# Kernel tuning notes

Hardware: AMD Instinct MI355X
Metric: run time of the kernel (lower is better)

Reference implementation:

```python
import jax, jax.numpy as jnp
import numpy as np


def setup_inputs() -> dict:
    key = jax.random.key(0)
    ks = jax.random.split(key, 6)
    b, t, k, h = 2, 2048, 256, 8
    s = 1.0 / np.sqrt(k)
    return {
        "x": jax.random.normal(ks[0], (b, t, k), dtype=jnp.float32),
        "Wq": jax.random.normal(ks[1], (k, k * h), dtype=jnp.float32) * s,
        "Wk": jax.random.normal(ks[2], (k, k * h), dtype=jnp.float32) * s,
        "Wv": jax.random.normal(ks[3], (k, k * h), dtype=jnp.float32) * s,
        "Wu": jax.random.normal(ks[4], (k * h, k), dtype=jnp.float32) * (1.0 / np.sqrt(k * h)),
        "bu": jnp.zeros((k,), dtype=jnp.float32),
    }


def reference(x, Wq, Wk, Wv, Wu, bu):
    b, t, k = x.shape
    h = Wq.shape[1] // k
    scale = k ** (-0.25)
    # projections -> [b, t, h, k] -> [b, h, t, k]
    q = (x @ Wq).reshape(b, t, h, k).transpose(0, 2, 1, 3) * scale
    kk = (x @ Wk).reshape(b, t, h, k).transpose(0, 2, 1, 3) * scale
    v = (x @ Wv).reshape(b, t, h, k).transpose(0, 2, 1, 3)
    dot = jnp.einsum('bhqk,bhsk->bhqs', q, kk)  # [b,h,t,t]
    attn = jax.nn.softmax(dot, axis=-1)
    out = jnp.einsum('bhqs,bhsk->bhqk', attn, v)  # [b,h,t,k]
    out = out.transpose(0, 2, 1, 3).reshape(b, t, h * k)
    return out @ Wu + bu
```

## Files before the change

kernel.cpp:

```cpp
#include <hip/hip_runtime.h>

using bf16x8   = __bf16 __attribute__((ext_vector_type(8)));
using floatx4  = float __attribute__((ext_vector_type(4)));
using floatx16 = float __attribute__((ext_vector_type(16)));

static __device__ __forceinline__ unsigned short f2b(float x) {
  unsigned u = __builtin_bit_cast(unsigned, x);
  u = (u + 0x7fffu + ((u >> 16) & 1u)) >> 16;
  return (unsigned short)u;
}

static __device__ __forceinline__ void gl_lds16(const unsigned short* g, unsigned short* l) {
  __builtin_amdgcn_global_load_lds((const __attribute__((address_space(1))) void*)g,
                                   (__attribute__((address_space(3))) void*)l, 16, 0, 0);
}

__global__ __launch_bounds__(256) void prep_kernel(const float* __restrict__ x,
                                                   const float* __restrict__ Wq,
                                                   const float* __restrict__ Wk,
                                                   const float* __restrict__ Wv,
                                                   const float* __restrict__ Wu,
                                                   unsigned short* __restrict__ xb,
                                                   unsigned short* __restrict__ wqkt,
                                                   unsigned short* __restrict__ wvt,
                                                   unsigned short* __restrict__ wut) {
  int bx = blockIdx.x;
  if (bx < 1024) {
    int i = (bx * 256 + threadIdx.x) * 4;
    float4 v = *(const float4*)(x + i);
    unsigned long long p = (unsigned long long)f2b(v.x) |
                           ((unsigned long long)f2b(v.y) << 16) |
                           ((unsigned long long)f2b(v.z) << 32) |
                           ((unsigned long long)f2b(v.w) << 48);
    *(unsigned long long*)(xb + i) = p;
    return;
  }
  __shared__ unsigned short T[64][65];
  const float* src;
  unsigned short* dst;
  int R, C, tile;
  if (bx < 1152)      { src = Wq; dst = wqkt;          R = 256;  C = 2048; tile = bx - 1024; }
  else if (bx < 1280) { src = Wk; dst = wqkt + 524288; R = 256;  C = 2048; tile = bx - 1152; }
  else if (bx < 1408) { src = Wv; dst = wvt;           R = 256;  C = 2048; tile = bx - 1280; }
  else                { src = Wu; dst = wut;           R = 2048; C = 256;  tile = bx - 1408; }
  int ctiles = C >> 6;
  int cx = tile % ctiles, ry = tile / ctiles;
  int r0 = ry * 64, c0 = cx * 64;
  int t = threadIdx.x;
#pragma unroll
  for (int i = 0; i < 16; ++i) {
    int idx = i * 256 + t;
    int r = idx >> 6, c = idx & 63;
    T[r][c] = f2b(src[(size_t)(r0 + r) * C + c0 + c]);
  }
  __syncthreads();
#pragma unroll
  for (int i = 0; i < 16; ++i) {
    int idx = i * 256 + t;
    int c = idx >> 6, r = idx & 63;
    dst[(size_t)(c0 + c) * R + r0 + r] = T[r][c];
  }
}

__global__ __launch_bounds__(256) void proj_kernel(const unsigned short* __restrict__ A,
                                                   const unsigned short* __restrict__ Bt,
                                                   unsigned short* __restrict__ qkb,
                                                   unsigned short* __restrict__ vtb) {
  __shared__ __align__(16) unsigned short SMEM[128 * 136];
  unsigned short* As = SMEM;
  unsigned short* Bs = SMEM + 4096;
  const int Kt = 256;
  int tid = threadIdx.x, lane = tid & 63, w = tid >> 6;
  int m16 = lane & 15, quad = lane >> 4;
  int wr = w & 1, wc = w >> 1;
  int m0 = blockIdx.y * 128, n0 = blockIdx.x * 128;
  int srow0 = w * 32 + (lane >> 2);
  int schunk = (lane & 3) ^ ((lane >> 2) & 3);
  floatx4 acc[4][4] = {};
  for (int k0 = 0; k0 < Kt; k0 += 32) {
    __syncthreads();
#pragma unroll
    for (int j = 0; j < 2; ++j) {
      int r = srow0 + j * 16;
      gl_lds16(A + (size_t)(m0 + r) * Kt + k0 + schunk * 8, &As[(w * 32 + j * 16) * 32]);
      gl_lds16(Bt + (size_t)(n0 + r) * Kt + k0 + schunk * 8, &Bs[(w * 32 + j * 16) * 32]);
    }
    __syncthreads();
    int sw = (quad ^ (m16 & 3)) * 8;
    bf16x8 af[4], bfr[4];
#pragma unroll
    for (int i = 0; i < 4; ++i) {
      af[i]  = *(const bf16x8*)(&As[(wr * 64 + i * 16 + m16) * 32 + sw]);
      bfr[i] = *(const bf16x8*)(&Bs[(wc * 64 + i * 16 + m16) * 32 + sw]);
    }
#pragma unroll
    for (int i = 0; i < 4; ++i)
#pragma unroll
      for (int jn = 0; jn < 4; ++jn)
        acc[i][jn] = __builtin_amdgcn_mfma_f32_16x16x32_bf16(af[i], bfr[jn], acc[i][jn], 0, 0, 0);
  }
  if (n0 < 4096) {
    float qscale = (n0 < 2048) ? 0.0625f : 1.0f;
#pragma unroll
    for (int i = 0; i < 4; ++i)
#pragma unroll
      for (int jn = 0; jn < 4; ++jn)
#pragma unroll
        for (int r = 0; r < 4; ++r) {
          int m = m0 + wr * 64 + i * 16 + quad * 4 + r;
          int n = n0 + wc * 64 + jn * 16 + m16;
          qkb[(size_t)m * 4096 + n] = f2b(acc[i][jn][r] * qscale);
        }
  } else {
    __syncthreads();
    unsigned short* Vt = SMEM;
#pragma unroll
    for (int i = 0; i < 4; ++i)
#pragma unroll
      for (int jn = 0; jn < 4; ++jn)
#pragma unroll
        for (int r = 0; r < 4; ++r) {
          int nn = wc * 64 + jn * 16 + m16;
          int mm = wr * 64 + i * 16 + quad * 4 + r;
          Vt[nn * 136 + mm] = f2b(acc[i][jn][r]);
        }
    __syncthreads();
    int bb = m0 >> 11, t0 = m0 & 2047;
#pragma unroll
    for (int i2 = 0; i2 < 8; ++i2) {
      int idx = i2 * 256 + tid;
      int nn = idx >> 4;
      int mc = (idx & 15) * 8;
      uint4 v = *(const uint4*)(&Vt[nn * 136 + mc]);
      *(uint4*)(&vtb[((size_t)(bb * 2048 + n0 - 4096 + nn)) * 2048 + t0 + mc]) = v;
    }
  }
}

__global__ __launch_bounds__(256) void out_kernel(const unsigned short* __restrict__ A,
                                                  const unsigned short* __restrict__ Bt,
                                                  float* __restrict__ Cout,
                                                  const float* __restrict__ bias) {
  __shared__ unsigned short As[64 * 128];
  __shared__ unsigned short Bs[64 * 128];
  const int Kt = 2048;
  int tid = threadIdx.x, lane = tid & 63, w = tid >> 6;
  int m16 = lane & 15, quad = lane >> 4;
  int m0 = blockIdx.y * 64, n0 = blockIdx.x * 64;
  int srow_i = lane >> 4;
  int spos = lane & 15;
  int rsw = m16 & 7;
  floatx4 acc[4] = {};
  for (int k0 = 0; k0 < Kt; k0 += 128) {
    __syncthreads();
#pragma unroll
    for (int j = 0; j < 4; ++j) {
      int r = w * 16 + j * 4 + srow_i;
      gl_lds16(A + (size_t)(m0 + r) * Kt + k0 + ((spos ^ (r & 7)) * 8), &As[(w * 16 + j * 4) * 128]);
      gl_lds16(Bt + (size_t)(n0 + r) * Kt + k0 + ((spos ^ (r & 7)) * 8), &Bs[(w * 16 + j * 4) * 128]);
    }
    __syncthreads();
    bf16x8 af[4];
#pragma unroll
    for (int kk = 0; kk < 4; ++kk)
      af[kk] = *(const bf16x8*)(&As[(w * 16 + m16) * 128 + (((kk * 4 + quad) ^ rsw) * 8)]);
#pragma unroll
    for (int nt = 0; nt < 4; ++nt)
#pragma unroll
      for (int kk = 0; kk < 4; ++kk) {
        bf16x8 bfv = *(const bf16x8*)(&Bs[(nt * 16 + m16) * 128 + (((kk * 4 + quad) ^ rsw) * 8)]);
        acc[nt] = __builtin_amdgcn_mfma_f32_16x16x32_bf16(af[kk], bfv, acc[nt], 0, 0, 0);
      }
  }
#pragma unroll
  for (int nt = 0; nt < 4; ++nt)
#pragma unroll
    for (int r = 0; r < 4; ++r) {
      int m = m0 + w * 16 + quad * 4 + r;
      int n = n0 + nt * 16 + m16;
      Cout[(size_t)m * 256 + n] = acc[nt][r] + bias[n];
    }
}

__global__ __launch_bounds__(512, 2) void attn_kernel(const unsigned short* __restrict__ qk,
                                                      const unsigned short* __restrict__ vt,
                                                      unsigned short* __restrict__ ao) {
  __shared__ __align__(16) unsigned short Ks[2][64 * 256];
  __shared__ __align__(16) unsigned short Vs[2][256 * 64];
  __shared__ __align__(16) unsigned short Pb[4][32 * 72];
  int tid = threadIdx.x, lane = tid & 63, w = tid >> 6;
  int c32 = lane & 31, hi = lane >> 5;
  int qg = w & 3, u = w >> 2;
  int id = blockIdx.x;
  int xcd = id & 7, j = id >> 3;
  int bh = xcd + 8 * (j & 1);
  int q0 = (j >> 1) * 128;
  int b = bh >> 3, h = bh & 7;

  bf16x8 qf[16];
  const unsigned short* qrow =
      qk + (size_t)(b * 2048 + q0 + qg * 32 + c32) * 4096 + h * 256 + hi * 8;
#pragma unroll
  for (int kk = 0; kk < 16; ++kk) qf[kk] = *(const bf16x8*)(qrow + kk * 16);

  bf16x8 onesf;
#pragma unroll
  for (int i = 0; i < 8; ++i) onesf[i] = (__bf16)1.0f;

  floatx16 O[4] = {};
  floatx16 l = {};

  const unsigned short* kbase = qk + (size_t)b * 2048 * 4096 + 2048 + h * 256;
  const unsigned short* vbase = vt + (size_t)bh * 256 * 2048;
  unsigned short* pq = &Pb[qg][0];

  int krow_i = lane >> 5, kpos = lane & 31;
  int vrow_i = lane >> 3, vpos = lane & 7;
  int ksw = c32 & 7;

#pragma unroll
  for (int i = 0; i < 4; ++i) {
    int kr = i * 2 + krow_i;
    gl_lds16(kbase + (size_t)(w * 8 + kr) * 4096 + ((kpos ^ (kr & 7)) * 8),
             &Ks[0][(w * 8 + i * 2) * 256]);
    int vr = i * 8 + vrow_i;
    gl_lds16(vbase + (size_t)(w * 32 + vr) * 2048 + ((vpos ^ vrow_i) * 8),
             &Vs[0][(w * 32 + i * 8) * 64]);
  }

  for (int st = 0; st < 32; ++st) {
    int cur = st & 1;
    __syncthreads();

    floatx16 s = {};
    const unsigned short* krl = &Ks[cur][(u * 32 + c32) * 256];
#pragma unroll
    for (int kk = 0; kk < 16; ++kk) {
      bf16x8 kf = *(const bf16x8*)(krl + (((kk * 2 + hi) ^ ksw) * 8));
      s = __builtin_amdgcn_mfma_f32_32x32x16_bf16(qf[kk], kf, s, 0, 0, 0);
    }
#pragma unroll
    for (int i = 0; i < 16; ++i) {
      float p = __expf(s[i]);
      int q = (i & 3) + 8 * (i >> 2) + 4 * hi;
      pq[q * 72 + u * 32 + c32] = f2b(p);
    }
    __syncthreads();

    if (st < 31) {
      int s0 = (st + 1) * 64;
      unsigned short* kdst = &Ks[1 - cur][0];
      unsigned short* vdst = &Vs[1 - cur][0];
#pragma unroll
      for (int i = 0; i < 4; ++i) {
        int kr = i * 2 + krow_i;
        gl_lds16(kbase + (size_t)(s0 + w * 8 + kr) * 4096 + ((kpos ^ (kr & 7)) * 8),
                 kdst + (w * 8 + i * 2) * 256);
        int vr = i * 8 + vrow_i;
        gl_lds16(vbase + (size_t)(w * 32 + vr) * 2048 + s0 + ((vpos ^ vrow_i) * 8),
                 vdst + (w * 32 + i * 8) * 64);
      }
    }

    bf16x8 paf[4];
#pragma unroll
    for (int f = 0; f < 4; ++f) paf[f] = *(const bf16x8*)(pq + c32 * 72 + f * 16 + hi * 8);
#pragma unroll
    for (int f = 0; f < 4; ++f)
      l = __builtin_amdgcn_mfma_f32_32x32x16_bf16(paf[f], onesf, l, 0, 0, 0);
#pragma unroll
    for (int dt = 0; dt < 4; ++dt) {
      const unsigned short* vrl = &Vs[cur][(u * 128 + dt * 32 + c32) * 64];
#pragma unroll
      for (int f = 0; f < 4; ++f) {
        bf16x8 vf = *(const bf16x8*)(vrl + (((f * 2 + hi) ^ ksw) * 8));
        O[dt] = __builtin_amdgcn_mfma_f32_32x32x16_bf16(paf[f], vf, O[dt], 0, 0, 0);
      }
    }
  }
  float inv[16];
#pragma unroll
  for (int i = 0; i < 16; ++i) inv[i] = 1.0f / l[i];
#pragma unroll
  for (int dt = 0; dt < 4; ++dt)
#pragma unroll
    for (int i = 0; i < 16; ++i) {
      int q = (i & 3) + 8 * (i >> 2) + 4 * hi;
      ao[(size_t)(b * 2048 + q0 + qg * 32 + q) * 2048 + h * 256 + u * 128 + dt * 32 + c32] =
          f2b(O[dt][i] * inv[i]);
    }
}

extern "C" void kernel_launch(void* const* d_in, const int* in_sizes, int n_in,
                              void* d_out, int out_size, void* d_ws, size_t ws_size,
                              hipStream_t stream) {
  const float* x  = (const float*)d_in[0];
  const float* Wq = (const float*)d_in[1];
  const float* Wk = (const float*)d_in[2];
  const float* Wv = (const float*)d_in[3];
  const float* Wu = (const float*)d_in[4];
  const float* bu = (const float*)d_in[5];

  unsigned short* xb   = (unsigned short*)d_ws;
  unsigned short* wqkt = xb + 1048576;
  unsigned short* wvt  = wqkt + 1048576;
  unsigned short* wut  = wvt + 524288;
  unsigned short* qkb  = wut + 524288;
  unsigned short* vtb  = qkb + 16777216;
  unsigned short* aob  = vtb + 8388608;

  prep_kernel<<<1536, 256, 0, stream>>>(x, Wq, Wk, Wv, Wu, xb, wqkt, wvt, wut);
  proj_kernel<<<dim3(48, 32), 256, 0, stream>>>(xb, wqkt, qkb, vtb);
  attn_kernel<<<256, 512, 0, stream>>>(qkb, vtb, aob);
  out_kernel<<<dim3(4, 64), 256, 0, stream>>>(aob, wut, (float*)d_out, bu);
}
```

Baseline: 193.7 us.

## Double-buffer LDS in projection/output GEMMs and compute softmax denominators with scalar sums

Both GEMM kernels now double-buffer the shared-memory tiles. The next k-slab is prefetched with global_load_lds while MFMAs run on the current slab, which removes one barrier per iteration. In the attention kernel, the row-sum MFMA against a ones vector is replaced by per-lane fp32 accumulation of the exponentials. This is followed by a cross-lane shuffle reduction and an LDS exchange between the two key-halves at the end. This drops 4 MFMAs per step and uses unrounded fp32 sums, at the cost of more LDS and extra final synchronisation.

New measurement: 191.6 us. No clear change (-1.1%).

```diff
diff --git a/kernel.cpp b/kernel.cpp
--- a/kernel.cpp
+++ b/kernel.cpp
@@ -67,8 +67,6 @@
                                                    unsigned short* __restrict__ qkb,
                                                    unsigned short* __restrict__ vtb) {
   __shared__ __align__(16) unsigned short SMEM[128 * 136];
-  unsigned short* As = SMEM;
-  unsigned short* Bs = SMEM + 4096;
   const int Kt = 256;
   int tid = threadIdx.x, lane = tid & 63, w = tid >> 6;
   int m16 = lane & 15, quad = lane >> 4;
@@ -77,15 +75,27 @@
   int srow0 = w * 32 + (lane >> 2);
   int schunk = (lane & 3) ^ ((lane >> 2) & 3);
   floatx4 acc[4][4] = {};
+#pragma unroll
+  for (int j = 0; j < 2; ++j) {
+    int r = srow0 + j * 16;
+    gl_lds16(A + (size_t)(m0 + r) * Kt + schunk * 8, &SMEM[(w * 32 + j * 16) * 32]);
+    gl_lds16(Bt + (size_t)(n0 + r) * Kt + schunk * 8, &SMEM[4096 + (w * 32 + j * 16) * 32]);
+  }
   for (int k0 = 0; k0 < Kt; k0 += 32) {
-    __syncthreads();
-#pragma unroll
-    for (int j = 0; j < 2; ++j) {
-      int r = srow0 + j * 16;
-      gl_lds16(A + (size_t)(m0 + r) * Kt + k0 + schunk * 8, &As[(w * 32 + j * 16) * 32]);
-      gl_lds16(Bt + (size_t)(n0 + r) * Kt + k0 + schunk * 8, &Bs[(w * 32 + j * 16) * 32]);
-    }
-    __syncthreads();
+    int cur = (k0 >> 5) & 1;
+    unsigned short* As = SMEM + cur * 8192;
+    unsigned short* Bs = As + 4096;
+    __syncthreads();
+    if (k0 + 32 < Kt) {
+      unsigned short* Ad = SMEM + (1 - cur) * 8192;
+      unsigned short* Bd = Ad + 4096;
+#pragma unroll
+      for (int j = 0; j < 2; ++j) {
+        int r = srow0 + j * 16;
+        gl_lds16(A + (size_t)(m0 + r) * Kt + k0 + 32 + schunk * 8, Ad + (w * 32 + j * 16) * 32);
+        gl_lds16(Bt + (size_t)(n0 + r) * Kt + k0 + 32 + schunk * 8, Bd + (w * 32 + j * 16) * 32);
+      }
+    }
     int sw = (quad ^ (m16 & 3)) * 8;
     bf16x8 af[4], bfr[4];
 #pragma unroll
@@ -141,8 +151,7 @@
                                                   const unsigned short* __restrict__ Bt,
                                                   float* __restrict__ Cout,
                                                   const float* __restrict__ bias) {
-  __shared__ unsigned short As[64 * 128];
-  __shared__ unsigned short Bs[64 * 128];
+  __shared__ __align__(16) unsigned short SMEM[32768];
   const int Kt = 2048;
   int tid = threadIdx.x, lane = tid & 63, w = tid >> 6;
   int m16 = lane & 15, quad = lane >> 4;
@@ -151,15 +160,29 @@
   int spos = lane & 15;
   int rsw = m16 & 7;
   floatx4 acc[4] = {};
+#pragma unroll
+  for (int j = 0; j < 4; ++j) {
+    int r = w * 16 + j * 4 + srow_i;
+    gl_lds16(A + (size_t)(m0 + r) * Kt + ((spos ^ (r & 7)) * 8), &SMEM[(w * 16 + j * 4) * 128]);
+    gl_lds16(Bt + (size_t)(n0 + r) * Kt + ((spos ^ (r & 7)) * 8), &SMEM[8192 + (w * 16 + j * 4) * 128]);
+  }
   for (int k0 = 0; k0 < Kt; k0 += 128) {
-    __syncthreads();
-#pragma unroll
-    for (int j = 0; j < 4; ++j) {
-      int r = w * 16 + j * 4 + srow_i;
-      gl_lds16(A + (size_t)(m0 + r) * Kt + k0 + ((spos ^ (r & 7)) * 8), &As[(w * 16 + j * 4) * 128]);
-      gl_lds16(Bt + (size_t)(n0 + r) * Kt + k0 + ((spos ^ (r & 7)) * 8), &Bs[(w * 16 + j * 4) * 128]);
-    }
-    __syncthreads();
+    int cur = (k0 >> 7) & 1;
+    unsigned short* As = SMEM + cur * 16384;
+    unsigned short* Bs = As + 8192;
+    __syncthreads();
+    if (k0 + 128 < Kt) {
+      unsigned short* Ad = SMEM + (1 - cur) * 16384;
+      unsigned short* Bd = Ad + 8192;
+#pragma unroll
+      for (int j = 0; j < 4; ++j) {
+        int r = w * 16 + j * 4 + srow_i;
+        gl_lds16(A + (size_t)(m0 + r) * Kt + k0 + 128 + ((spos ^ (r & 7)) * 8),
+                 Ad + (w * 16 + j * 4) * 128);
+        gl_lds16(Bt + (size_t)(n0 + r) * Kt + k0 + 128 + ((spos ^ (r & 7)) * 8),
+                 Bd + (w * 16 + j * 4) * 128);
+      }
+    }
     bf16x8 af[4];
 #pragma unroll
     for (int kk = 0; kk < 4; ++kk)
@@ -203,12 +226,8 @@
 #pragma unroll
   for (int kk = 0; kk < 16; ++kk) qf[kk] = *(const bf16x8*)(qrow + kk * 16);
 
-  bf16x8 onesf;
-#pragma unroll
-  for (int i = 0; i < 8; ++i) onesf[i] = (__bf16)1.0f;
-
   floatx16 O[4] = {};
-  floatx16 l = {};
+  floatx16 lacc = {};
 
   const unsigned short* kbase = qk + (size_t)b * 2048 * 4096 + 2048 + h * 256;
   const unsigned short* vbase = vt + (size_t)bh * 256 * 2048;
@@ -242,6 +261,7 @@
 #pragma unroll
     for (int i = 0; i < 16; ++i) {
       float p = __expf(s[i]);
+      lacc[i] += p;
       int q = (i & 3) + 8 * (i >> 2) + 4 * hi;
       pq[q * 72 + u * 32 + c32] = f2b(p);
     }
@@ -266,9 +286,6 @@
 #pragma unroll
     for (int f = 0; f < 4; ++f) paf[f] = *(const bf16x8*)(pq + c32 * 72 + f * 16 + hi * 8);
 #pragma unroll
-    for (int f = 0; f < 4; ++f)
-      l = __builtin_amdgcn_mfma_f32_32x32x16_bf16(paf[f], onesf, l, 0, 0, 0);
-#pragma unroll
     for (int dt = 0; dt < 4; ++dt) {
       const unsigned short* vrl = &Vs[cur][(u * 128 + dt * 32 + c32) * 64];
 #pragma unroll
@@ -278,16 +295,29 @@
       }
     }
   }
-  float inv[16];
-#pragma unroll
-  for (int i = 0; i < 16; ++i) inv[i] = 1.0f / l[i];
-#pragma unroll
-  for (int dt = 0; dt < 4; ++dt)
+
+#pragma unroll
+  for (int off = 1; off < 32; off <<= 1)
+#pragma unroll
+    for (int i = 0; i < 16; ++i) lacc[i] += __shfl_xor(lacc[i], off);
+  float* lsh = (float*)&Ks[0][0];
+  __syncthreads();
+  if (c32 == 0) {
 #pragma unroll
     for (int i = 0; i < 16; ++i) {
       int q = (i & 3) + 8 * (i >> 2) + 4 * hi;
+      lsh[u * 128 + qg * 32 + q] = lacc[i];
+    }
+  }
+  __syncthreads();
+#pragma unroll
+  for (int dt = 0; dt < 4; ++dt)
+#pragma unroll
+    for (int i = 0; i < 16; ++i) {
+      int q = (i & 3) + 8 * (i >> 2) + 4 * hi;
+      float lr = 1.0f / (lsh[qg * 32 + q] + lsh[128 + qg * 32 + q]);
       ao[(size_t)(b * 2048 + q0 + qg * 32 + q) * 2048 + h * 256 + u * 128 + dt * 32 + c32] =
-          f2b(O[dt][i] * inv[i]);
+          f2b(O[dt][i] * lr);
     }
 }
 
```
